# Kernel optimization log

Hardware: AMD Instinct MI355X
Metric: run time of the kernel (lower is better)

## Reference

```python
import jax, jax.numpy as jnp
import numpy as np

N_QUBITS = 4
DIM = 16
N_QLAYERS = 2

def _cnot_perm(c, t):
    idx = np.arange(DIM)
    cbit = (idx >> (N_QUBITS - 1 - c)) & 1
    return np.where(cbit == 1, idx ^ (1 << (N_QUBITS - 1 - t)), idx)

# ring entanglement: CNOT(0,1), CNOT(1,2), CNOT(2,3), CNOT(3,0)
RING_PERMS = [jnp.asarray(_cnot_perm(i, (i + 1) % N_QUBITS)) for i in range(N_QUBITS)]
_idx = np.arange(DIM)
ZSIGNS = jnp.asarray(np.stack([1.0 - 2.0 * ((_idx >> (N_QUBITS - 1 - q)) & 1) for q in range(N_QUBITS)], axis=1).astype(np.float32))  # (16, 4)

def _rx(t):
    c = jnp.cos(t / 2).astype(jnp.complex64)
    s = jnp.sin(t / 2).astype(jnp.complex64)
    return jnp.stack([jnp.stack([c, -1j * s]), jnp.stack([-1j * s, c])])

def _ry(t):
    c = jnp.cos(t / 2).astype(jnp.complex64)
    s = jnp.sin(t / 2).astype(jnp.complex64)
    return jnp.stack([jnp.stack([c, -s]), jnp.stack([s, c])])

def _rz(t):
    e = jnp.exp(-0.5j * t.astype(jnp.complex64))
    z = jnp.zeros((), jnp.complex64)
    return jnp.stack([jnp.stack([e, z]), jnp.stack([z, jnp.conj(e)])])

def _apply_1q(state, g, q):
    # wire 0 is the most significant bit (PennyLane convention)
    s = state.reshape(2 ** q, 2, 2 ** (N_QUBITS - 1 - q))
    return jnp.einsum('ij,ajc->aic', g, s).reshape(DIM)

def _circuit(angles, qw):
    # angles: (4,), qw: (n_qlayers, 4, 3); returns PauliZ expvals (4,)
    state = jnp.zeros(DIM, jnp.complex64).at[0].set(1.0)
    for q in range(N_QUBITS):
        state = _apply_1q(state, _ry(angles[q]), q)
    for l in range(N_QLAYERS):
        for q in range(N_QUBITS):
            state = _apply_1q(state, _rx(qw[l, q, 0]), q)
            state = _apply_1q(state, _ry(qw[l, q, 1]), q)
            state = _apply_1q(state, _rz(qw[l, q, 2]), q)
        for p in RING_PERMS:
            state = state[p]
    probs = jnp.abs(state) ** 2
    return probs @ ZSIGNS

def _conv(x, w, b, stride, pad):
    y = jax.lax.conv_general_dilated(x, w, (stride, stride), [(pad, pad), (pad, pad)], dimension_numbers=('NCHW', 'OIHW', 'NCHW'))
    return y + b[None, :, None, None]

def _bn(x, g, b, m, v):
    scale = (g / jnp.sqrt(v + 1e-5))[None, :, None, None]
    return (x - m[None, :, None, None]) * scale + b[None, :, None, None]

def _forward(x, c1w, c1b, bn1g, bn1b, bn1m, bn1v, c2w, c2b, bn2g, bn2b, bn2m, bn2v, c3w, c3b, bn3g, bn3b, bn3m, bn3v, pre_w, pre_b, qw, pw1, pb1, pw2, pb2):
    B = x.shape[0]
    h = jax.nn.relu(_bn(_conv(x, c1w, c1b, 4, 3), bn1g, bn1b, bn1m, bn1v))   # (B,32,56,56)
    h = jax.nn.relu(_bn(_conv(h, c2w, c2b, 2, 1), bn2g, bn2b, bn2m, bn2v))   # (B,64,28,28)
    h = jax.nn.relu(_bn(_conv(h, c3w, c3b, 2, 1), bn3g, bn3b, bn3m, bn3v))   # (B,128,14,14)
    h = h.reshape(B, 128, 2, 7, 2, 7).mean(axis=(3, 5))                       # AdaptiveAvgPool2d((2,2))
    f = h.reshape(B, 128 * 4)
    ang = jnp.tanh(f @ pre_w.T + pre_b) * jnp.pi                              # (B,4)
    qout = jax.vmap(lambda a: _circuit(a, qw))(ang)                            # (B,4) batched statevector sim
    h1 = jax.nn.relu(qout @ pw1.T + pb1)                                       # dropout inactive (eval)
    return h1 @ pw2.T + pb2

def setup_inputs() -> dict:
    key = jax.random.key(0)
    ks = jax.random.split(key, 16)
    d = {
        'x': jax.random.normal(ks[0], (128, 3, 224, 224), jnp.float32),
        'c1w': jax.random.normal(ks[1], (32, 3, 7, 7), jnp.float32) * 0.05,
        'c1b': jax.random.normal(ks[2], (32,), jnp.float32) * 0.05,
        'bn1g': jnp.ones((32,), jnp.float32), 'bn1b': jnp.zeros((32,), jnp.float32),
        'bn1m': jnp.zeros((32,), jnp.float32), 'bn1v': jnp.ones((32,), jnp.float32),
        'c2w': jax.random.normal(ks[3], (64, 32, 3, 3), jnp.float32) * 0.05,
        'c2b': jax.random.normal(ks[4], (64,), jnp.float32) * 0.05,
        'bn2g': jnp.ones((64,), jnp.float32), 'bn2b': jnp.zeros((64,), jnp.float32),
        'bn2m': jnp.zeros((64,), jnp.float32), 'bn2v': jnp.ones((64,), jnp.float32),
        'c3w': jax.random.normal(ks[5], (128, 64, 3, 3), jnp.float32) * 0.05,
        'c3b': jax.random.normal(ks[6], (128,), jnp.float32) * 0.05,
        'bn3g': jnp.ones((128,), jnp.float32), 'bn3b': jnp.zeros((128,), jnp.float32),
        'bn3m': jnp.zeros((128,), jnp.float32), 'bn3v': jnp.ones((128,), jnp.float32),
        'pre_w': jax.random.normal(ks[7], (4, 512), jnp.float32) * 0.04,
        'pre_b': jax.random.normal(ks[8], (4,), jnp.float32) * 0.04,
        'qw': jax.random.normal(ks[9], (2, 4, 3), jnp.float32) * 0.1,
        'pw1': jax.random.normal(ks[10], (64, 4), jnp.float32) * 0.5,
        'pb1': jax.random.normal(ks[11], (64,), jnp.float32) * 0.5,
        'pw2': jax.random.normal(ks[12], (5, 64), jnp.float32) * 0.12,
        'pb2': jax.random.normal(ks[13], (5,), jnp.float32) * 0.12,
    }
    return d

def reference(x, c1w, c1b, bn1g, bn1b, bn1m, bn1v, c2w, c2b, bn2g, bn2b, bn2m, bn2v, c3w, c3b, bn3g, bn3b, bn3m, bn3v, pre_w, pre_b, qw, pw1, pb1, pw2, pb2):
    return _forward(x, c1w, c1b, bn1g, bn1b, bn1m, bn1v, c2w, c2b, bn2g, bn2b, bn2m, bn2v, c3w, c3b, bn3g, bn3b, bn3m, bn3v, pre_w, pre_b, qw, pw1, pb1, pw2, pb2)
```

## Files before the change

kernel.cpp:

```cpp
#include <hip/hip_runtime.h>
#include <math.h>

#define DEV __device__ __forceinline__

typedef __attribute__((ext_vector_type(8))) __bf16 bf16x8;
typedef __attribute__((ext_vector_type(4))) float f32x4;

__global__ void prep_all(
    const float* __restrict__ x, long nx8,
    const float* __restrict__ c1w, const float* __restrict__ c1b,
    const float* __restrict__ g1, const float* __restrict__ b1,
    const float* __restrict__ m1, const float* __restrict__ v1,
    const float* __restrict__ c2w, const float* __restrict__ c2b,
    const float* __restrict__ g2, const float* __restrict__ b2,
    const float* __restrict__ m2, const float* __restrict__ v2,
    const float* __restrict__ c3w, const float* __restrict__ c3b,
    const float* __restrict__ g3, const float* __restrict__ b3,
    const float* __restrict__ m3, const float* __restrict__ v3,
    __bf16* __restrict__ xpad,
    __bf16* __restrict__ wb1, __bf16* __restrict__ wb2, __bf16* __restrict__ wb3,
    float* __restrict__ sc1, float* __restrict__ sh1,
    float* __restrict__ sc2, float* __restrict__ sh2,
    float* __restrict__ sc3, float* __restrict__ sh3)
{
    long gid = (long)blockIdx.x * 256 + threadIdx.x;
    long gs = (long)gridDim.x * 256;
    const float4* x4 = (const float4*)x;
    bf16x8* xp8 = (bf16x8*)xpad;
    for (long e = gid; e < nx8; e += gs) {
        float4 a = x4[2 * e], b = x4[2 * e + 1];
        bf16x8 o;
        o[0] = (__bf16)a.x; o[1] = (__bf16)a.y; o[2] = (__bf16)a.z; o[3] = (__bf16)a.w;
        o[4] = (__bf16)b.x; o[5] = (__bf16)b.y; o[6] = (__bf16)b.z; o[7] = (__bf16)b.w;
        xp8[e] = o;
    }

    for (long e = gid; e < 32 * 192; e += gs) {
        int oc = e / 192, k = e % 192, rr = k >> 3, kw = k & 7;
        wb1[e] = (rr < 21 && kw >= 1) ? (__bf16)c1w[oc * 147 + rr * 7 + kw - 1]
                                      : (__bf16)0.f;
    }
    for (long e = gid; e < 64 * 384; e += gs) {
        int oc = e / 384, k = e % 384, rr = k >> 2, kw = k & 3;
        wb2[e] = (kw >= 1) ? (__bf16)c2w[oc * 288 + rr * 3 + kw - 1] : (__bf16)0.f;
    }
    for (long e = gid; e < 128 * 768; e += gs) {
        int oc = e / 768, k = e % 768, rr = k >> 2, kw = k & 3;
        wb3[e] = (kw >= 1) ? (__bf16)c3w[oc * 576 + rr * 3 + kw - 1] : (__bf16)0.f;
    }
    if (gid < 32) {
        float s = g1[gid] * rsqrtf(v1[gid] + 1e-5f);
        sc1[gid] = s; sh1[gid] = (c1b[gid] - m1[gid]) * s + b1[gid];
    } else if (gid < 96) {
        int i = gid - 32;
        float s = g2[i] * rsqrtf(v2[i] + 1e-5f);
        sc2[i] = s; sh2[i] = (c2b[i] - m2[i]) * s + b2[i];
    } else if (gid < 224) {
        int i = gid - 96;
        float s = g3[i] * rsqrtf(v3[i] + 1e-5f);
        sc3[i] = s; sh3[i] = (c3b[i] - m3[i]) * s + b3[i];
    }
}

template<typename OUTT, int IC, int KS, int RW, int S, int P,
         int IH, int IW, int OH, int OW, int OC, int KTP, int KOFF, int KCH,
         bool EPI>
DEV void conv_body(
    const __bf16* __restrict__ xo,
    const __bf16* __restrict__ wb,
    const float* __restrict__ scale,
    const float* __restrict__ shift,
    OUTT* __restrict__ out,
    __bf16* Is, __bf16* Ws)
{
    constexpr int KITER = KCH / 32;
    static_assert(KCH % 32 == 0, "KCH");
    constexpr int OHW = OH * OW;
    constexpr int IHW = IH * IW;
    constexpr int LDR = 40;
    constexpr int NROW = 16 / RW;
    constexpr int RU = RW / 2;

    const int tid = threadIdx.x;
    const int sb0 = blockIdx.x * 128;
    const int oc0 = blockIdx.y * 32;

    const int sm = tid & 127;
    const int kpb = tid >> 7;
    int a_n, a_ih0, a_iw0;
    {
        int m = sb0 + sm;
        a_n = m / OHW;
        int rem = m % OHW;
        a_ih0 = (rem / OW) * S - P;
        a_iw0 = (rem % OW) * S - P;
    }
    unsigned ihok = 0;
    #pragma unroll
    for (int t = 0; t < KS; ++t)
        ihok |= (unsigned)(((a_ih0 + t) >= 0) && ((a_ih0 + t) < IH)) << t;
    const bool left = (a_iw0 < 0);
    const __bf16* xp = xo + ((size_t)a_n * IC * IHW + (ptrdiff_t)a_ih0 * IW
                             + (a_iw0 - 1));

    const int w_oc = tid >> 2;
    const int w_j  = tid & 3;

    const int wave = tid >> 6, lane = tid & 63;
    const int quad = lane >> 4, l16 = lane & 15;

    f32x4 acc[2][2] = {};

    #pragma unroll
    for (int ci = 0; ci < KITER; ++ci) {
        const int k0 = KOFF + ci * 32;

        union { unsigned u[8]; bf16x8 v[2]; } Pk;
        #pragma unroll
        for (int r = 0; r < NROW; ++r) {
            const int rr = (k0 / RW) + kpb * NROW + r;
            if (rr >= IC * KS) {
                #pragma unroll
                for (int q = 0; q < RU; ++q) Pk.u[r * RU + q] = 0u;
            } else {
                const int ic = rr / KS, kh = rr % KS;
                const unsigned* rp = (const unsigned*)(xp + (ic * IHW + kh * IW));
                unsigned t[RU];
                #pragma unroll
                for (int q = 0; q < RU; ++q) t[q] = rp[q];
                bool rok = (ihok >> kh) & 1u;
                #pragma unroll
                for (int q = 0; q < RU; ++q) t[q] = rok ? t[q] : 0u;
                t[0] = left ? (t[0] & 0x0000FFFFu) : t[0];
                if constexpr (P >= 2) t[1] = left ? 0u : t[1];
                #pragma unroll
                for (int q = 0; q < RU; ++q) Pk.u[r * RU + q] = t[q];
            }
        }
        bf16x8 wv = {};
        if (tid < 128)
            wv = *(const bf16x8*)&wb[(size_t)(oc0 + w_oc) * KTP + k0 + w_j * 8];

        __syncthreads();
        *(bf16x8*)&Is[sm * LDR + kpb * 16]     = Pk.v[0];
        *(bf16x8*)&Is[sm * LDR + kpb * 16 + 8] = Pk.v[1];
        if (tid < 128) *(bf16x8*)&Ws[w_oc * LDR + w_j * 8] = wv;
        __syncthreads();

        bf16x8 afr[2], bfr[2];
        #pragma unroll
        for (int mt = 0; mt < 2; ++mt)
            afr[mt] = *(const bf16x8*)&Ws[(mt * 16 + l16) * LDR + quad * 8];
        #pragma unroll
        for (int nt = 0; nt < 2; ++nt)
            bfr[nt] = *(const bf16x8*)&Is[(wave * 32 + nt * 16 + l16) * LDR + quad * 8];
        #pragma unroll
        for (int mt = 0; mt < 2; ++mt)
            #pragma unroll
            for (int nt = 0; nt < 2; ++nt)
                acc[mt][nt] = __builtin_amdgcn_mfma_f32_16x16x32_bf16(
                    afr[mt], bfr[nt], acc[mt][nt], 0, 0, 0);
    }

    #pragma unroll
    for (int mt = 0; mt < 2; ++mt) {
        #pragma unroll
        for (int r = 0; r < 4; ++r) {
            int oc = oc0 + mt * 16 + quad * 4 + r;
            float scl = EPI ? scale[oc] : 0.f;
            float shf = EPI ? shift[oc] : 0.f;
            #pragma unroll
            for (int nt = 0; nt < 2; ++nt) {
                int sg = sb0 + wave * 32 + nt * 16 + l16;
                int n = sg / OHW, s = sg % OHW;
                float v = acc[mt][nt][r];
                if (EPI) {
                    v = fmaf(v, scl, shf);
                    v = v > 0.f ? v : 0.f;
                }
                out[((size_t)n * OC + oc) * OHW + s] = (OUTT)v;
            }
        }
    }
}

template<typename OUTT, int IC, int KS, int RW, int S, int P,
         int IH, int IW, int OH, int OW, int OC, int KTP, int KCH, bool EPI>
__global__ __launch_bounds__(256, 6) void conv_mfma_kernel(
    const __bf16* __restrict__ xo, const __bf16* __restrict__ wb,
    const float* __restrict__ scale, const float* __restrict__ shift,
    OUTT* __restrict__ out)
{
    __shared__ __attribute__((aligned(16))) __bf16 Is[128 * 40];
    __shared__ __attribute__((aligned(16))) __bf16 Ws[32 * 40];
    conv_body<OUTT, IC, KS, RW, S, P, IH, IW, OH, OW, OC, KTP, 0, KCH, EPI>(
        xo, wb, scale, shift, out, Is, Ws);
}

__global__ __launch_bounds__(256, 6) void conv3_kernel(
    const __bf16* __restrict__ xo, const __bf16* __restrict__ wb,
    float* __restrict__ p3a, float* __restrict__ p3b)
{
    __shared__ __attribute__((aligned(16))) __bf16 Is[128 * 40];
    __shared__ __attribute__((aligned(16))) __bf16 Ws[32 * 40];
    if (blockIdx.z == 0)
        conv_body<float, 64, 3, 4, 2, 1, 28, 28, 14, 14, 128, 768, 0, 384, false>(
            xo, wb, nullptr, nullptr, p3a, Is, Ws);
    else
        conv_body<float, 64, 3, 4, 2, 1, 28, 28, 14, 14, 128, 768, 384, 384, false>(
            xo, wb, nullptr, nullptr, p3b, Is, Ws);
}

__global__ __launch_bounds__(256) void pool_bn_kernel(
    const float* __restrict__ p3a, const float* __restrict__ p3b,
    const float* __restrict__ sc3, const float* __restrict__ sh3,
    float* __restrict__ f)
{
    int idx = blockIdx.x * 256 + threadIdx.x;
    int b = idx >> 9, p = idx & 511;
    int c = p >> 2, i = (p >> 1) & 1, j = p & 1;
    size_t base = ((size_t)b * 128 + c) * 196 + (i * 7) * 14 + j * 7;
    float scl = sc3[c], shf = sh3[c];
    float s = 0.f;
    #pragma unroll
    for (int u = 0; u < 7; ++u)
        #pragma unroll
        for (int v = 0; v < 7; ++v) {
            size_t k = base + u * 14 + v;
            float val = fmaf(p3a[k] + p3b[k], scl, shf);
            s += val > 0.f ? val : 0.f;
        }
    f[idx] = s * (1.f / 49.f);
}

DEV void gate_ry(float* re, float* im, int q, float th) {
    float c = cosf(th * 0.5f), s = sinf(th * 0.5f);
    int mask = 8 >> q;
    for (int i = 0; i < 16; ++i) {
        if (i & mask) continue;
        int j = i | mask;
        float r0 = re[i], i0 = im[i], r1 = re[j], i1 = im[j];
        re[i] = c * r0 - s * r1;  im[i] = c * i0 - s * i1;
        re[j] = s * r0 + c * r1;  im[j] = s * i0 + c * i1;
    }
}
DEV void gate_rx(float* re, float* im, int q, float th) {
    float c = cosf(th * 0.5f), s = sinf(th * 0.5f);
    int mask = 8 >> q;
    for (int i = 0; i < 16; ++i) {
        if (i & mask) continue;
        int j = i | mask;
        float r0 = re[i], i0 = im[i], r1 = re[j], i1 = im[j];
        re[i] = c * r0 + s * i1;  im[i] = c * i0 - s * r1;
        re[j] = s * i0 + c * r1;  im[j] = -s * r0 + c * i1;
    }
}
DEV void gate_rz(float* re, float* im, int q, float th) {
    float c = cosf(th * 0.5f), s = sinf(th * 0.5f);
    int mask = 8 >> q;
    for (int i = 0; i < 16; ++i) {
        float sg = (i & mask) ? s : -s;
        float r = re[i], m = im[i];
        re[i] = c * r - sg * m;
        im[i] = c * m + sg * r;
    }
}
DEV void gate_cnot(float* re, float* im, int c, int t) {
    int cm = 8 >> c, tm = 8 >> t;
    for (int i = 0; i < 16; ++i) {
        if ((i & cm) && !(i & tm)) {
            int j = i | tm;
            float r = re[i]; re[i] = re[j]; re[j] = r;
            float m = im[i]; im[i] = im[j]; im[j] = m;
        }
    }
}

__global__ __launch_bounds__(256) void head_kernel(
    const float* __restrict__ fpool,
    const float* __restrict__ pre_w, const float* __restrict__ pre_b,
    const float* __restrict__ qw,
    const float* __restrict__ pw1, const float* __restrict__ pb1,
    const float* __restrict__ pw2, const float* __restrict__ pb2,
    float* __restrict__ out)
{
    __shared__ float f[512];
    __shared__ float ang[4];
    __shared__ float sre[16], simg[16];
    __shared__ float zexp[4];
    __shared__ float h1[64];

    int b = blockIdx.x;
    int t = threadIdx.x;

    for (int p = t; p < 512; p += 256) f[p] = fpool[b * 512 + p];
    __syncthreads();

    int wv = t >> 6, lane = t & 63;
    float partial = 0.f;
    for (int d = lane; d < 512; d += 64)
        partial += f[d] * pre_w[wv * 512 + d];
    #pragma unroll
    for (int off = 32; off > 0; off >>= 1)
        partial += __shfl_down(partial, off, 64);
    if (lane == 0)
        ang[wv] = tanhf(partial + pre_b[wv]) * 3.14159265358979323846f;
    __syncthreads();

    if (t == 0) {
        for (int i = 0; i < 16; ++i) { sre[i] = 0.f; simg[i] = 0.f; }
        sre[0] = 1.f;
        for (int q = 0; q < 4; ++q) gate_ry(sre, simg, q, ang[q]);
        for (int l = 0; l < 2; ++l) {
            for (int q = 0; q < 4; ++q) {
                const float* qq = qw + (l * 4 + q) * 3;
                gate_rx(sre, simg, q, qq[0]);
                gate_ry(sre, simg, q, qq[1]);
                gate_rz(sre, simg, q, qq[2]);
            }
            gate_cnot(sre, simg, 0, 1);
            gate_cnot(sre, simg, 1, 2);
            gate_cnot(sre, simg, 2, 3);
            gate_cnot(sre, simg, 3, 0);
        }
        for (int q = 0; q < 4; ++q) {
            float z = 0.f;
            for (int i = 0; i < 16; ++i) {
                float p2 = sre[i] * sre[i] + simg[i] * simg[i];
                z += (((i >> (3 - q)) & 1) ? -p2 : p2);
            }
            zexp[q] = z;
        }
    }
    __syncthreads();

    if (t < 64) {
        float s = pb1[t];
        #pragma unroll
        for (int k = 0; k < 4; ++k) s += zexp[k] * pw1[t * 4 + k];
        h1[t] = s > 0.f ? s : 0.f;
    }
    __syncthreads();

    if (t < 5) {
        float s = pb2[t];
        for (int k = 0; k < 64; ++k) s += h1[k] * pw2[t * 64 + k];
        out[b * 5 + t] = s;
    }
}

extern "C" void kernel_launch(void* const* d_in, const int* in_sizes, int n_in,
                              void* d_out, int out_size, void* d_ws, size_t ws_size,
                              hipStream_t stream) {
    const float* x    = (const float*)d_in[0];
    const float* c1w  = (const float*)d_in[1];
    const float* c1b  = (const float*)d_in[2];
    const float* bn1g = (const float*)d_in[3];
    const float* bn1b = (const float*)d_in[4];
    const float* bn1m = (const float*)d_in[5];
    const float* bn1v = (const float*)d_in[6];
    const float* c2w  = (const float*)d_in[7];
    const float* c2b  = (const float*)d_in[8];
    const float* bn2g = (const float*)d_in[9];
    const float* bn2b = (const float*)d_in[10];
    const float* bn2m = (const float*)d_in[11];
    const float* bn2v = (const float*)d_in[12];
    const float* c3w  = (const float*)d_in[13];
    const float* c3bi = (const float*)d_in[14];
    const float* bn3g = (const float*)d_in[15];
    const float* bn3b = (const float*)d_in[16];
    const float* bn3m = (const float*)d_in[17];
    const float* bn3v = (const float*)d_in[18];
    const float* prw  = (const float*)d_in[19];
    const float* prb  = (const float*)d_in[20];
    const float* qw   = (const float*)d_in[21];
    const float* pw1  = (const float*)d_in[22];
    const float* pb1  = (const float*)d_in[23];
    const float* pw2  = (const float*)d_in[24];
    const float* pb2  = (const float*)d_in[25];

    const int N = in_sizes[0] / (3 * 224 * 224);
    const long NX  = (long)N * 3 * 224 * 224;
    const size_t NC1 = (size_t)N * 32 * 56 * 56;
    const size_t NC2 = (size_t)N * 64 * 28 * 28;

    __bf16* ws_h = (__bf16*)d_ws;
    __bf16* xpad_alloc = ws_h;
    __bf16* xpad = xpad_alloc + 1024;
    __bf16* c1o_alloc = xpad_alloc + 1024 + NX + 64;
    __bf16* c1o = c1o_alloc + 64;
    __bf16* c2o_alloc = c1o_alloc + 64 + NC1 + 64;
    __bf16* c2o = c2o_alloc + 64;
    __bf16* wb1 = c2o_alloc + 64 + NC2 + 64;
    __bf16* wb2 = wb1 + 32 * 192;
    __bf16* wb3 = wb2 + 64 * 384;
    float* sc1 = (float*)(wb3 + 128 * 768);
    float* sh1 = sc1 + 32;
    float* sc2 = sh1 + 32;  float* sh2 = sc2 + 64;
    float* sc3 = sh2 + 64;  float* sh3 = sc3 + 128;
    float* fpool = sh3 + 128;
    float* p3a = (float*)xpad_alloc;
    float* p3b = p3a + (size_t)N * 128 * 14 * 14;

    prep_all<<<1024, 256, 0, stream>>>(
        x, NX / 8,
        c1w, c1b, bn1g, bn1b, bn1m, bn1v,
        c2w, c2b, bn2g, bn2b, bn2m, bn2v,
        c3w, c3bi, bn3g, bn3b, bn3m, bn3v,
        xpad, wb1, wb2, wb3, sc1, sh1, sc2, sh2, sc3, sh3);

    conv_mfma_kernel<__bf16, 3, 7, 8, 4, 3, 224, 224, 56, 56, 32, 192, 192, true>
        <<<dim3(401408 / 128, 1), 256, 0, stream>>>(xpad, wb1, sc1, sh1, c1o);
    conv_mfma_kernel<__bf16, 32, 3, 4, 2, 1, 56, 56, 28, 28, 64, 384, 384, true>
        <<<dim3(100352 / 128, 2), 256, 0, stream>>>(c1o, wb2, sc2, sh2, c2o);
    conv3_kernel<<<dim3(25088 / 128, 4, 2), 256, 0, stream>>>(c2o, wb3, p3a, p3b);

    pool_bn_kernel<<<(N * 512) / 256, 256, 0, stream>>>(p3a, p3b, sc3, sh3, fpool);
    head_kernel<<<N, 256, 0, stream>>>(fpool, prw, prb, qw,
                                       pw1, pb1, pw2, pb2, (float*)d_out);
}
```

Measured before the change: 250.9 us.

## Fuse input bf16 conversion into conv1, widen conv2 tile, drop conv3 split-K

```diff
diff --git a/kernel.cpp b/kernel.cpp
--- a/kernel.cpp
+++ b/kernel.cpp
@@ -6,8 +6,7 @@
 typedef __attribute__((ext_vector_type(8))) __bf16 bf16x8;
 typedef __attribute__((ext_vector_type(4))) float f32x4;
 
-__global__ void prep_all(
-    const float* __restrict__ x, long nx8,
+__global__ void prep_weights(
     const float* __restrict__ c1w, const float* __restrict__ c1b,
     const float* __restrict__ g1, const float* __restrict__ b1,
     const float* __restrict__ m1, const float* __restrict__ v1,
@@ -17,34 +16,23 @@
     const float* __restrict__ c3w, const float* __restrict__ c3b,
     const float* __restrict__ g3, const float* __restrict__ b3,
     const float* __restrict__ m3, const float* __restrict__ v3,
-    __bf16* __restrict__ xpad,
     __bf16* __restrict__ wb1, __bf16* __restrict__ wb2, __bf16* __restrict__ wb3,
     float* __restrict__ sc1, float* __restrict__ sh1,
     float* __restrict__ sc2, float* __restrict__ sh2,
     float* __restrict__ sc3, float* __restrict__ sh3)
 {
-    long gid = (long)blockIdx.x * 256 + threadIdx.x;
-    long gs = (long)gridDim.x * 256;
-    const float4* x4 = (const float4*)x;
-    bf16x8* xp8 = (bf16x8*)xpad;
-    for (long e = gid; e < nx8; e += gs) {
-        float4 a = x4[2 * e], b = x4[2 * e + 1];
-        bf16x8 o;
-        o[0] = (__bf16)a.x; o[1] = (__bf16)a.y; o[2] = (__bf16)a.z; o[3] = (__bf16)a.w;
-        o[4] = (__bf16)b.x; o[5] = (__bf16)b.y; o[6] = (__bf16)b.z; o[7] = (__bf16)b.w;
-        xp8[e] = o;
-    }
-
-    for (long e = gid; e < 32 * 192; e += gs) {
+    int gid = blockIdx.x * 256 + threadIdx.x;
+    int gs = gridDim.x * 256;
+    for (int e = gid; e < 32 * 192; e += gs) {
         int oc = e / 192, k = e % 192, rr = k >> 3, kw = k & 7;
         wb1[e] = (rr < 21 && kw >= 1) ? (__bf16)c1w[oc * 147 + rr * 7 + kw - 1]
                                       : (__bf16)0.f;
     }
-    for (long e = gid; e < 64 * 384; e += gs) {
+    for (int e = gid; e < 64 * 384; e += gs) {
         int oc = e / 384, k = e % 384, rr = k >> 2, kw = k & 3;
         wb2[e] = (kw >= 1) ? (__bf16)c2w[oc * 288 + rr * 3 + kw - 1] : (__bf16)0.f;
     }
-    for (long e = gid; e < 128 * 768; e += gs) {
+    for (int e = gid; e < 128 * 768; e += gs) {
         int oc = e / 768, k = e % 768, rr = k >> 2, kw = k & 3;
         wb3[e] = (kw >= 1) ? (__bf16)c3w[oc * 576 + rr * 3 + kw - 1] : (__bf16)0.f;
     }
@@ -62,19 +50,122 @@
     }
 }
 
-template<typename OUTT, int IC, int KS, int RW, int S, int P,
-         int IH, int IW, int OH, int OW, int OC, int KTP, int KOFF, int KCH,
-         bool EPI>
+__global__ __launch_bounds__(256, 6) void conv1_kernel(
+    const float* __restrict__ x,
+    const __bf16* __restrict__ wb,
+    const float* __restrict__ scale, const float* __restrict__ shift,
+    __bf16* __restrict__ out)
+{
+    constexpr int IHW = 224 * 224, OHW = 56 * 56, LDR = 40;
+    __shared__ __attribute__((aligned(16))) __bf16 Is[128 * LDR];
+    __shared__ __attribute__((aligned(16))) __bf16 Ws[32 * LDR];
+
+    const int tid = threadIdx.x;
+    const int sb0 = blockIdx.x * 128;
+    const int sm = tid & 127;
+    const int kpb = tid >> 7;
+
+    int a_n, a_ih0, a_iw0;
+    {
+        int m = sb0 + sm;
+        a_n = m / OHW;
+        int rem = m % OHW;
+        a_ih0 = (rem / 56) * 4 - 3;
+        a_iw0 = (rem % 56) * 4 - 3;
+    }
+    unsigned ihok = 0;
+    #pragma unroll
+    for (int t = 0; t < 7; ++t)
+        ihok |= (unsigned)(((a_ih0 + t) >= 0) && ((a_ih0 + t) < 224)) << t;
+    const bool left = (a_iw0 < 0);
+    const int boff = a_n * 3 * IHW + a_ih0 * 224 + (a_iw0 - 1);
+
+    const int w_oc = tid >> 2, w_j = tid & 3;
+    const int wave = tid >> 6, lane = tid & 63;
+    const int quad = lane >> 4, l16 = lane & 15;
+
+    f32x4 acc[2][2] = {};
+
+    #pragma unroll
+    for (int ci = 0; ci < 6; ++ci) {
+        const int k0 = ci * 32;
+        bf16x8 hv[2];
+        #pragma unroll
+        for (int r = 0; r < 2; ++r) {
+            const int rr = ci * 4 + kpb * 2 + r;
+            if (rr >= 21) {
+                hv[r] = (bf16x8){};
+            } else {
+                const int ic = rr / 7, kh = rr % 7;
+                int off = boff + (ic * IHW + kh * 224);
+                int o0 = off < 0 ? 0 : off;
+                int o1 = (off + 4) < 0 ? 0 : (off + 4);
+                float4 A = *(const float4*)(x + o0);
+                float4 B = *(const float4*)(x + o1);
+                float va[8] = {A.x, A.y, A.z, A.w, B.x, B.y, B.z, B.w};
+                bool rok = (ihok >> kh) & 1u;
+                #pragma unroll
+                for (int j = 0; j < 8; ++j) va[j] = rok ? va[j] : 0.f;
+                #pragma unroll
+                for (int j = 1; j <= 3; ++j) va[j] = left ? 0.f : va[j];
+                bf16x8 h;
+                #pragma unroll
+                for (int j = 0; j < 8; ++j) h[j] = (__bf16)va[j];
+                hv[r] = h;
+            }
+        }
+        bf16x8 wv = {};
+        if (tid < 128)
+            wv = *(const bf16x8*)&wb[(size_t)w_oc * 192 + k0 + w_j * 8];
+
+        __syncthreads();
+        *(bf16x8*)&Is[sm * LDR + kpb * 16]     = hv[0];
+        *(bf16x8*)&Is[sm * LDR + kpb * 16 + 8] = hv[1];
+        if (tid < 128) *(bf16x8*)&Ws[w_oc * LDR + w_j * 8] = wv;
+        __syncthreads();
+
+        bf16x8 afr[2], bfr[2];
+        #pragma unroll
+        for (int mt = 0; mt < 2; ++mt)
+            afr[mt] = *(const bf16x8*)&Ws[(mt * 16 + l16) * LDR + quad * 8];
+        #pragma unroll
+        for (int nt = 0; nt < 2; ++nt)
+            bfr[nt] = *(const bf16x8*)&Is[(wave * 32 + nt * 16 + l16) * LDR + quad * 8];
+        #pragma unroll
+        for (int mt = 0; mt < 2; ++mt)
+            #pragma unroll
+            for (int nt = 0; nt < 2; ++nt)
+                acc[mt][nt] = __builtin_amdgcn_mfma_f32_16x16x32_bf16(
+                    afr[mt], bfr[nt], acc[mt][nt], 0, 0, 0);
+    }
+
+    #pragma unroll
+    for (int mt = 0; mt < 2; ++mt) {
+        #pragma unroll
+        for (int r = 0; r < 4; ++r) {
+            int oc = mt * 16 + quad * 4 + r;
+            float scl = scale[oc], shf = shift[oc];
+            #pragma unroll
+            for (int nt = 0; nt < 2; ++nt) {
+                int sg = sb0 + wave * 32 + nt * 16 + l16;
+                int n = sg / OHW, s = sg % OHW;
+                float v = fmaf(acc[mt][nt][r], scl, shf);
+                v = v > 0.f ? v : 0.f;
+                out[((size_t)n * 32 + oc) * OHW + s] = (__bf16)v;
+            }
+        }
+    }
+}
+
+template<typename OUTT, int NOCT, int IC, int KS, int RW, int S, int P,
+         int IH, int IW, int OH, int OW, int OC, int KTP, int KCH, bool EPI>
 DEV void conv_body(
     const __bf16* __restrict__ xo,
     const __bf16* __restrict__ wb,
-    const float* __restrict__ scale,
-    const float* __restrict__ shift,
-    OUTT* __restrict__ out,
-    __bf16* Is, __bf16* Ws)
+    const float* __restrict__ scale, const float* __restrict__ shift,
+    OUTT* __restrict__ out, __bf16* Is, __bf16* Ws)
 {
     constexpr int KITER = KCH / 32;
-    static_assert(KCH % 32 == 0, "KCH");
     constexpr int OHW = OH * OW;
     constexpr int IHW = IH * IW;
     constexpr int LDR = 40;
@@ -83,7 +174,7 @@
 
     const int tid = threadIdx.x;
     const int sb0 = blockIdx.x * 128;
-    const int oc0 = blockIdx.y * 32;
+    const int oc0 = blockIdx.y * (NOCT * 16);
 
     const int sm = tid & 127;
     const int kpb = tid >> 7;
@@ -103,17 +194,15 @@
     const __bf16* xp = xo + ((size_t)a_n * IC * IHW + (ptrdiff_t)a_ih0 * IW
                              + (a_iw0 - 1));
 
-    const int w_oc = tid >> 2;
-    const int w_j  = tid & 3;
-
+    const int w_oc = tid >> 2, w_j = tid & 3;
     const int wave = tid >> 6, lane = tid & 63;
     const int quad = lane >> 4, l16 = lane & 15;
 
-    f32x4 acc[2][2] = {};
+    f32x4 acc[NOCT][2] = {};
 
     #pragma unroll
     for (int ci = 0; ci < KITER; ++ci) {
-        const int k0 = KOFF + ci * 32;
+        const int k0 = ci * 32;
 
         union { unsigned u[8]; bf16x8 v[2]; } Pk;
         #pragma unroll
@@ -138,24 +227,24 @@
             }
         }
         bf16x8 wv = {};
-        if (tid < 128)
+        if (NOCT == 4 || tid < 128)
             wv = *(const bf16x8*)&wb[(size_t)(oc0 + w_oc) * KTP + k0 + w_j * 8];
 
         __syncthreads();
         *(bf16x8*)&Is[sm * LDR + kpb * 16]     = Pk.v[0];
         *(bf16x8*)&Is[sm * LDR + kpb * 16 + 8] = Pk.v[1];
-        if (tid < 128) *(bf16x8*)&Ws[w_oc * LDR + w_j * 8] = wv;
+        if (NOCT == 4 || tid < 128) *(bf16x8*)&Ws[w_oc * LDR + w_j * 8] = wv;
         __syncthreads();
 
-        bf16x8 afr[2], bfr[2];
-        #pragma unroll
-        for (int mt = 0; mt < 2; ++mt)
+        bf16x8 afr[NOCT], bfr[2];
+        #pragma unroll
+        for (int mt = 0; mt < NOCT; ++mt)
             afr[mt] = *(const bf16x8*)&Ws[(mt * 16 + l16) * LDR + quad * 8];
         #pragma unroll
         for (int nt = 0; nt < 2; ++nt)
             bfr[nt] = *(const bf16x8*)&Is[(wave * 32 + nt * 16 + l16) * LDR + quad * 8];
         #pragma unroll
-        for (int mt = 0; mt < 2; ++mt)
+        for (int mt = 0; mt < NOCT; ++mt)
             #pragma unroll
             for (int nt = 0; nt < 2; ++nt)
                 acc[mt][nt] = __builtin_amdgcn_mfma_f32_16x16x32_bf16(
@@ -163,7 +252,7 @@
     }
 
     #pragma unroll
-    for (int mt = 0; mt < 2; ++mt) {
+    for (int mt = 0; mt < NOCT; ++mt) {
         #pragma unroll
         for (int r = 0; r < 4; ++r) {
             int oc = oc0 + mt * 16 + quad * 4 + r;
@@ -184,52 +273,42 @@
     }
 }
 
-template<typename OUTT, int IC, int KS, int RW, int S, int P,
-         int IH, int IW, int OH, int OW, int OC, int KTP, int KCH, bool EPI>
-__global__ __launch_bounds__(256, 6) void conv_mfma_kernel(
+__global__ __launch_bounds__(256, 4) void conv2_kernel(
     const __bf16* __restrict__ xo, const __bf16* __restrict__ wb,
     const float* __restrict__ scale, const float* __restrict__ shift,
-    OUTT* __restrict__ out)
+    __bf16* __restrict__ out)
+{
+    __shared__ __attribute__((aligned(16))) __bf16 Is[128 * 40];
+    __shared__ __attribute__((aligned(16))) __bf16 Ws[64 * 40];
+    conv_body<__bf16, 4, 32, 3, 4, 2, 1, 56, 56, 28, 28, 64, 384, 384, true>(
+        xo, wb, scale, shift, out, Is, Ws);
+}
+
+__global__ __launch_bounds__(256, 6) void conv3_kernel(
+    const __bf16* __restrict__ xo, const __bf16* __restrict__ wb,
+    const float* __restrict__ scale, const float* __restrict__ shift,
+    __bf16* __restrict__ out)
 {
     __shared__ __attribute__((aligned(16))) __bf16 Is[128 * 40];
     __shared__ __attribute__((aligned(16))) __bf16 Ws[32 * 40];
-    conv_body<OUTT, IC, KS, RW, S, P, IH, IW, OH, OW, OC, KTP, 0, KCH, EPI>(
+    conv_body<__bf16, 2, 64, 3, 4, 2, 1, 28, 28, 14, 14, 128, 768, 768, true>(
         xo, wb, scale, shift, out, Is, Ws);
 }
 
-__global__ __launch_bounds__(256, 6) void conv3_kernel(
-    const __bf16* __restrict__ xo, const __bf16* __restrict__ wb,
-    float* __restrict__ p3a, float* __restrict__ p3b)
-{
-    __shared__ __attribute__((aligned(16))) __bf16 Is[128 * 40];
-    __shared__ __attribute__((aligned(16))) __bf16 Ws[32 * 40];
-    if (blockIdx.z == 0)
-        conv_body<float, 64, 3, 4, 2, 1, 28, 28, 14, 14, 128, 768, 0, 384, false>(
-            xo, wb, nullptr, nullptr, p3a, Is, Ws);
-    else
-        conv_body<float, 64, 3, 4, 2, 1, 28, 28, 14, 14, 128, 768, 384, 384, false>(
-            xo, wb, nullptr, nullptr, p3b, Is, Ws);
-}
-
-__global__ __launch_bounds__(256) void pool_bn_kernel(
-    const float* __restrict__ p3a, const float* __restrict__ p3b,
-    const float* __restrict__ sc3, const float* __restrict__ sh3,
+__global__ __launch_bounds__(256) void pool_kernel(
+    const __bf16* __restrict__ c3o,
     float* __restrict__ f)
 {
     int idx = blockIdx.x * 256 + threadIdx.x;
     int b = idx >> 9, p = idx & 511;
     int c = p >> 2, i = (p >> 1) & 1, j = p & 1;
     size_t base = ((size_t)b * 128 + c) * 196 + (i * 7) * 14 + j * 7;
-    float scl = sc3[c], shf = sh3[c];
     float s = 0.f;
     #pragma unroll
     for (int u = 0; u < 7; ++u)
         #pragma unroll
-        for (int v = 0; v < 7; ++v) {
-            size_t k = base + u * 14 + v;
-            float val = fmaf(p3a[k] + p3b[k], scl, shf);
-            s += val > 0.f ? val : 0.f;
-        }
+        for (int v = 0; v < 7; ++v)
+            s += (float)c3o[base + u * 14 + v];
     f[idx] = s * (1.f / 49.f);
 }
 
@@ -380,18 +459,15 @@
     const float* pb2  = (const float*)d_in[25];
 
     const int N = in_sizes[0] / (3 * 224 * 224);
-    const long NX  = (long)N * 3 * 224 * 224;
     const size_t NC1 = (size_t)N * 32 * 56 * 56;
     const size_t NC2 = (size_t)N * 64 * 28 * 28;
+    const size_t NC3 = (size_t)N * 128 * 14 * 14;
 
     __bf16* ws_h = (__bf16*)d_ws;
-    __bf16* xpad_alloc = ws_h;
-    __bf16* xpad = xpad_alloc + 1024;
-    __bf16* c1o_alloc = xpad_alloc + 1024 + NX + 64;
-    __bf16* c1o = c1o_alloc + 64;
-    __bf16* c2o_alloc = c1o_alloc + 64 + NC1 + 64;
-    __bf16* c2o = c2o_alloc + 64;
-    __bf16* wb1 = c2o_alloc + 64 + NC2 + 64;
+    __bf16* c1o = ws_h + 64;
+    __bf16* c2o = ws_h + 64 + NC1 + 64 + 64;
+    __bf16* c3o = ws_h + 64 + NC1 + 64 + 64 + NC2 + 64;
+    __bf16* wb1 = c3o + NC3;
     __bf16* wb2 = wb1 + 32 * 192;
     __bf16* wb3 = wb2 + 64 * 384;
     float* sc1 = (float*)(wb3 + 128 * 768);
@@ -399,23 +475,18 @@
     float* sc2 = sh1 + 32;  float* sh2 = sc2 + 64;
     float* sc3 = sh2 + 64;  float* sh3 = sc3 + 128;
     float* fpool = sh3 + 128;
-    float* p3a = (float*)xpad_alloc;
-    float* p3b = p3a + (size_t)N * 128 * 14 * 14;
-
-    prep_all<<<1024, 256, 0, stream>>>(
-        x, NX / 8,
+
+    prep_weights<<<192, 256, 0, stream>>>(
         c1w, c1b, bn1g, bn1b, bn1m, bn1v,
         c2w, c2b, bn2g, bn2b, bn2m, bn2v,
         c3w, c3bi, bn3g, bn3b, bn3m, bn3v,
-        xpad, wb1, wb2, wb3, sc1, sh1, sc2, sh2, sc3, sh3);
-
-    conv_mfma_kernel<__bf16, 3, 7, 8, 4, 3, 224, 224, 56, 56, 32, 192, 192, true>
-        <<<dim3(401408 / 128, 1), 256, 0, stream>>>(xpad, wb1, sc1, sh1, c1o);
-    conv_mfma_kernel<__bf16, 32, 3, 4, 2, 1, 56, 56, 28, 28, 64, 384, 384, true>
-        <<<dim3(100352 / 128, 2), 256, 0, stream>>>(c1o, wb2, sc2, sh2, c2o);
-    conv3_kernel<<<dim3(25088 / 128, 4, 2), 256, 0, stream>>>(c2o, wb3, p3a, p3b);
-
-    pool_bn_kernel<<<(N * 512) / 256, 256, 0, stream>>>(p3a, p3b, sc3, sh3, fpool);
+        wb1, wb2, wb3, sc1, sh1, sc2, sh2, sc3, sh3);
+
+    conv1_kernel<<<dim3(401408 / 128, 1), 256, 0, stream>>>(x, wb1, sc1, sh1, c1o);
+    conv2_kernel<<<dim3(100352 / 128, 1), 256, 0, stream>>>(c1o, wb2, sc2, sh2, c2o);
+    conv3_kernel<<<dim3(25088 / 128, 4), 256, 0, stream>>>(c2o, wb3, sc3, sh3, c3o);
+
+    pool_kernel<<<(N * 512) / 256, 256, 0, stream>>>(c3o, fpool);
     head_kernel<<<N, 256, 0, stream>>>(fpool, prw, prb, qw,
                                        pw1, pb1, pw2, pb2, (float*)d_out);
 }
```

Result: faster. 245.1 us (-2.3%).
